# Optimization experiments

Measured on AMD Instinct MI355X. Metric: run time of the kernel, lower is better.

## Reference

```python
import jax, jax.numpy as jnp
import numpy as np

B, S, D, H = 256, 128, 1024, 8
DH = D // H  # per-head dim = input_length / head


def setup_inputs() -> dict:
    key = jax.random.key(0)
    ks = jax.random.split(key, 12)
    code = jax.random.normal(ks[0], (B, S, D), dtype=jnp.float32)
    # 0/1 adjacency (PDG relation mask)
    input_relation = jax.random.bernoulli(ks[1], 0.2, (B, S, S)).astype(jnp.float32)
    w = 0.02
    Wq = jax.random.normal(ks[2], (H, D, DH), dtype=jnp.float32) * w
    bq = jnp.zeros((H, DH), dtype=jnp.float32)
    Wk = jax.random.normal(ks[3], (H, D, DH), dtype=jnp.float32) * w
    bk = jnp.zeros((H, DH), dtype=jnp.float32)
    Wv = jax.random.normal(ks[4], (H, D, DH), dtype=jnp.float32) * w
    bv = jnp.zeros((H, DH), dtype=jnp.float32)
    Wo = jax.random.normal(ks[5], (2 * D, D), dtype=jnp.float32) * w
    bo = jnp.zeros((D,), dtype=jnp.float32)
    return {"code": code, "input_relation": input_relation,
            "Wq": Wq, "bq": bq, "Wk": Wk, "bk": bk,
            "Wv": Wv, "bv": bv, "Wo": Wo, "bo": bo}


def reference(code, input_relation, Wq, bq, Wk, bk, Wv, bv, Wo, bo):
    Hn = Wq.shape[0]
    half = Hn // 2
    Sn = code.shape[1]
    E = jnp.eye(Sn, dtype=code.dtype)
    # Faithful to the TF loop: head i < H/2 sees relation + i*I (the loop
    # reassigns input_relation = this_relation + I each iteration);
    # heads i >= H/2 see the ORIGINAL transposed relation.
    i_idx = jnp.arange(half, dtype=code.dtype)  # [half]
    rel_fwd = input_relation[None] + i_idx[:, None, None, None] * E  # [half,B,S,S]
    rel_t = jnp.swapaxes(input_relation, 1, 2)
    rel_bwd = jnp.broadcast_to(rel_t[None], (Hn - half,) + rel_t.shape)
    rels = jnp.concatenate([rel_fwd, rel_bwd], axis=0)  # [H,B,S,S]

    relu = jax.nn.relu
    Q = relu(jnp.einsum('bsd,hdf->hbsf', code, Wq) + bq[:, None, None, :])
    K = relu(jnp.einsum('bsd,hdf->hbsf', code, Wk) + bk[:, None, None, :])
    V = relu(jnp.einsum('bsd,hdf->hbsf', code, Wv) + bv[:, None, None, :])

    attn = jnp.einsum('hbsf,hbtf->hbst', Q, K)  # [H,B,S,S]
    pdg = rels * attn + 1e-11
    # tf.reduce_sum axis=1 (rows) -> our axis=2; axis=2 (cols) -> our axis=3
    indeg = jnp.sqrt(jnp.sum(pdg, axis=2, keepdims=True))   # [H,B,1,S]
    outdeg = jnp.sqrt(jnp.sum(pdg, axis=3, keepdims=True))  # [H,B,S,1]
    pdg = pdg / indeg / outdeg
    softed = rels * pdg
    res = jnp.einsum('hbst,hbtf->hbsf', softed, V)  # [H,B,S,DH]

    # concat heads along features (head 0 first), then concat original code
    all_ch = jnp.transpose(res, (1, 2, 0, 3)).reshape(code.shape[0], Sn, -1)
    add_ori = jnp.concatenate([all_ch, code], axis=-1)  # [B,S,2D]
    out = relu(add_ori @ Wo + bo)
    return out
```

## Files before the change

kernel.cpp:

```cpp
#include <hip/hip_runtime.h>
#include <cstdint>
#include <cstddef>

#define B_  256
#define S_  128
#define D_  1024
#define H_  8
#define DH_ 128
#define M_  (B_ * S_)

typedef _Float16 half8 __attribute__((ext_vector_type(8)));
typedef float    f32x4 __attribute__((ext_vector_type(4)));

#define GLOAD_LDS16(gp, lp)                                                    \
    __builtin_amdgcn_global_load_lds(                                          \
        (const __attribute__((address_space(1))) void*)(gp),                   \
        (__attribute__((address_space(3))) void*)(lp), 16, 0, 0)

__global__ __launch_bounds__(256)
void cvt_code(const float* __restrict__ src, _Float16* __restrict__ dst, int n8)
{
    int i = blockIdx.x * 256 + threadIdx.x;
    if (i >= n8) return;
    const float4* s = (const float4*)src;
    float4 a = s[2 * i], b = s[2 * i + 1];
    half8 o;
    o[0] = (_Float16)a.x; o[1] = (_Float16)a.y; o[2] = (_Float16)a.z; o[3] = (_Float16)a.w;
    o[4] = (_Float16)b.x; o[5] = (_Float16)b.y; o[6] = (_Float16)b.z; o[7] = (_Float16)b.w;
    *(half8*)(dst + (size_t)i * 8) = o;
}

__global__ __launch_bounds__(256)
void cvt_wqkv(const float* __restrict__ Wq, const float* __restrict__ Wk,
              const float* __restrict__ Wv,
              const float* __restrict__ bq, const float* __restrict__ bk,
              const float* __restrict__ bv,
              _Float16* __restrict__ Wt, float* __restrict__ bias_all)
{
    int idx = blockIdx.x * 256 + threadIdx.x;
    if (idx >= 3072 * 128) return;
    int n = idx >> 7, kc = idx & 127, k = kc * 8;
    int qkv = n >> 10, hf = n & 1023, h = hf >> 7, f = hf & 127;
    const float* W = (qkv == 0 ? Wq : (qkv == 1 ? Wk : Wv))
                     + (size_t)h * D_ * DH_ + (size_t)k * DH_ + f;
    half8 o;
    #pragma unroll
    for (int j = 0; j < 8; ++j) o[j] = (_Float16)W[(size_t)j * DH_];
    *(half8*)(Wt + (size_t)n * 1024 + k) = o;
    if (kc == 0)
        bias_all[n] = (qkv == 0 ? bq : (qkv == 1 ? bk : bv))[h * DH_ + f];
}

__global__ __launch_bounds__(256)
void cvt_wo(const float* __restrict__ Wo, _Float16* __restrict__ Wot)
{
    int idx = blockIdx.x * 256 + threadIdx.x;
    if (idx >= 1024 * 256) return;
    int n = idx >> 8, kc = idx & 255, k = kc * 8;
    const float* W = Wo + (size_t)k * 1024 + n;
    half8 o;
    #pragma unroll
    for (int j = 0; j < 8; ++j) o[j] = (_Float16)W[(size_t)j * 1024];
    *(half8*)(Wot + (size_t)n * 2048 + k) = o;
}

template <bool OUTF32>
__global__ __launch_bounds__(512, 1)
void gemm_f16_8p(const _Float16* __restrict__ A1p, const _Float16* __restrict__ A2p,
                 int K1, const _Float16* __restrict__ Bt,
                 const float* __restrict__ bias, void* __restrict__ outp,
                 int Ntot, int Ktot, int ntn)
{
    __shared__ __align__(16) char lds[131072];

    const int tid = threadIdx.x;
    const int w = tid >> 6, l = tid & 63;
    const int wm = w >> 2, wn = w & 3;
    const int lr = l & 15, lg = l >> 4;

    const int cpx = gridDim.x >> 3;
    const int bid = blockIdx.x;
    const int swz = (bid & 7) * cpx + (bid >> 3);
    const int m0 = (swz / ntn) * 256, n0 = (swz % ntn) * 256;

    const int NT = Ktot >> 6;

    const int srow  = l >> 3;
    const int sgcol = ((l & 7) ^ srow) * 8;

    auto stageHalf = [&](int bufi, int t, int half) {
        const int k0 = t << 6;
        const bool isA = (half == 0) || (half == 3);
        const int hh = (half >= 2) ? 1 : 0;
        char* dst0 = lds + bufi * 65536 + (isA ? 0 : 32768) + hh * 16384;
        if (isA) {
            const _Float16* Asrc; int kc;
            if (k0 < K1) { Asrc = A1p; kc = k0; } else { Asrc = A2p; kc = k0 - K1; }
            #pragma unroll
            for (int i = 0; i < 2; ++i) {
                const int c = i * 8 + w;
                const int row = hh * 128 + c * 8 + srow;
                const _Float16* g = Asrc + (size_t)(m0 + row) * 1024 + kc + sgcol;
                GLOAD_LDS16(g, dst0 + c * 1024);
            }
        } else {
            #pragma unroll
            for (int i = 0; i < 2; ++i) {
                const int c = i * 8 + w;
                const int row = hh * 128 + c * 8 + srow;
                const _Float16* g = Bt + (size_t)(n0 + row) * Ktot + k0 + sgcol;
                GLOAD_LDS16(g, dst0 + c * 1024);
            }
        }
    };

    auto ldA = [&](int bufi, int fi, int ks) -> half8 {
        const int row = fi * 32 + wm * 16 + lr;
        const int pos = (ks * 4 + lg) ^ (row & 7);
        return *(const half8*)(lds + bufi * 65536 + row * 128 + pos * 16);
    };
    auto ldB = [&](int bufi, int fj, int ks) -> half8 {
        const int row = fj * 64 + wn * 16 + lr;
        const int pos = (ks * 4 + lg) ^ (row & 7);
        return *(const half8*)(lds + bufi * 65536 + 32768 + row * 128 + pos * 16);
    };

    f32x4 acc[8][4] = {};
    half8 aq[4][2], b0[2][2], b1[2][2];

    stageHalf(0, 0, 0); stageHalf(0, 0, 1); stageHalf(0, 0, 2); stageHalf(0, 0, 3);

    for (int t = 0; t < NT; ++t) {
        const int buf = t & 1;
        const bool nl = (t + 1 < NT);

        asm volatile("s_waitcnt vmcnt(0)" ::: "memory");
        __builtin_amdgcn_s_barrier();

        if (nl) {
            stageHalf(buf ^ 1, t + 1, 0); stageHalf(buf ^ 1, t + 1, 1);
            stageHalf(buf ^ 1, t + 1, 2); stageHalf(buf ^ 1, t + 1, 3);
        }

        #pragma unroll
        for (int fi = 0; fi < 4; ++fi)
            #pragma unroll
            for (int ks = 0; ks < 2; ++ks)
                aq[fi][ks] = ldA(buf, fi, ks);
        #pragma unroll
        for (int fj = 0; fj < 2; ++fj)
            #pragma unroll
            for (int ks = 0; ks < 2; ++ks)
                b0[fj][ks] = ldB(buf, fj, ks);
        #pragma unroll
        for (int fj = 0; fj < 2; ++fj)
            #pragma unroll
            for (int ks = 0; ks < 2; ++ks)
                b1[fj][ks] = ldB(buf, fj + 2, ks);

        __builtin_amdgcn_s_setprio(1);
        #pragma unroll
        for (int ks = 0; ks < 2; ++ks)
            #pragma unroll
            for (int fi = 0; fi < 4; ++fi)
                #pragma unroll
                for (int fj = 0; fj < 2; ++fj)
                    acc[fi][fj] = __builtin_amdgcn_mfma_f32_16x16x32_f16(
                        aq[fi][ks], b0[fj][ks], acc[fi][fj], 0, 0, 0);
        #pragma unroll
        for (int ks = 0; ks < 2; ++ks)
            #pragma unroll
            for (int fi = 0; fi < 4; ++fi)
                #pragma unroll
                for (int fj = 0; fj < 2; ++fj)
                    acc[fi][fj + 2] = __builtin_amdgcn_mfma_f32_16x16x32_f16(
                        aq[fi][ks], b1[fj][ks], acc[fi][fj + 2], 0, 0, 0);
        __builtin_amdgcn_s_setprio(0);

        __builtin_amdgcn_s_barrier();

        #pragma unroll
        for (int fi = 0; fi < 4; ++fi)
            #pragma unroll
            for (int ks = 0; ks < 2; ++ks)
                aq[fi][ks] = ldA(buf, fi + 4, ks);

        __builtin_amdgcn_s_setprio(1);
        #pragma unroll
        for (int ks = 0; ks < 2; ++ks)
            #pragma unroll
            for (int fi = 0; fi < 4; ++fi)
                #pragma unroll
                for (int fj = 0; fj < 2; ++fj)
                    acc[fi + 4][fj + 2] = __builtin_amdgcn_mfma_f32_16x16x32_f16(
                        aq[fi][ks], b1[fj][ks], acc[fi + 4][fj + 2], 0, 0, 0);
        #pragma unroll
        for (int ks = 0; ks < 2; ++ks)
            #pragma unroll
            for (int fi = 0; fi < 4; ++fi)
                #pragma unroll
                for (int fj = 0; fj < 2; ++fj)
                    acc[fi + 4][fj] = __builtin_amdgcn_mfma_f32_16x16x32_f16(
                        aq[fi][ks], b0[fj][ks], acc[fi + 4][fj], 0, 0, 0);
        __builtin_amdgcn_s_setprio(0);
    }

    #pragma unroll
    for (int fi = 0; fi < 8; ++fi) {
        #pragma unroll
        for (int fj = 0; fj < 4; ++fj) {
            const int n = n0 + fj * 64 + wn * 16 + lr;
            const float bs = bias[n];
            #pragma unroll
            for (int rg = 0; rg < 4; ++rg) {
                const int m = m0 + fi * 32 + wm * 16 + lg * 4 + rg;
                float v = acc[fi][fj][rg] + bs;
                v = v > 0.0f ? v : 0.0f;
                if constexpr (OUTF32)
                    ((float*)outp)[(size_t)m * Ntot + n] = v;
                else
                    ((_Float16*)outp)[(size_t)m * Ntot + n] = (_Float16)v;
            }
        }
    }
}

__global__ __launch_bounds__(256, 2)
void attn_pdg_mfma(const _Float16* __restrict__ QKV, const float* __restrict__ Rel,
                   _Float16* __restrict__ resh)
{
    __shared__ __align__(16) char smem[75776];
    unsigned* rbits = (unsigned*)(smem + 70656);
    float* rowpart  = (float*)(smem + 72704);
    float* colpart  = (float*)(smem + 73728);
    float* inv_in   = (float*)(smem + 74752);
    float* inv_out  = (float*)(smem + 75264);

    const int tid = threadIdx.x;
    const int w = tid >> 6, l = tid & 63;
    const int wr = w >> 1, wc = w & 1;
    const int lr = l & 15, lg = l >> 4;
    const int h = blockIdx.x, b = blockIdx.y;

    for (int s = w; s < S_; s += 4) {
        const float* row = &Rel[((size_t)b * S_ + s) * S_];
        unsigned long long b0m = __ballot(row[l] > 0.5f);
        unsigned long long b1m = __ballot(row[64 + l] > 0.5f);
        if (l == 0) {
            rbits[s * 4 + 0] = (unsigned)b0m; rbits[s * 4 + 1] = (unsigned)(b0m >> 32);
            rbits[s * 4 + 2] = (unsigned)b1m; rbits[s * 4 + 3] = (unsigned)(b1m >> 32);
        }
    }

    const size_t gbase = (size_t)(b * S_) * 3072 + h * DH_;

    const _Float16* Vb = QKV + gbase + 2048;
    const int vrow = tid >> 1, vcol0 = (tid & 1) * 64;
    uint4 vreg[8];
    #pragma unroll
    for (int j = 0; j < 8; ++j)
        vreg[j] = *(const uint4*)&Vb[(size_t)vrow * 3072 + vcol0 + j * 8];

    #pragma unroll
    for (int i = 0; i < 8; ++i) {
        const int row = (w * 8 + i) * 4 + (l >> 4);
        const int gsrc = (l & 15) ^ (row & 7);
        const _Float16* gq = QKV + gbase + (size_t)row * 3072 + gsrc * 8;
        GLOAD_LDS16(gq, smem + (w * 8 + i) * 1024);
        const _Float16* gk = QKV + gbase + 1024 + (size_t)row * 3072 + gsrc * 8;
        GLOAD_LDS16(gk, smem + 32768 + (w * 8 + i) * 1024);
    }
    __syncthreads();

    f32x4 acc[4][4] = {};
    #pragma unroll
    for (int kc = 0; kc < 4; ++kc) {
        half8 af[4], bf[4];
        #pragma unroll
        for (int i = 0; i < 4; ++i) {
            const int row = wr * 64 + i * 16 + lr;
            const int pos = (kc * 4 + lg) ^ (row & 7);
            af[i] = *(const half8*)(smem + row * 256 + pos * 16);
        }
        #pragma unroll
        for (int j = 0; j < 4; ++j) {
            const int row = wc * 64 + j * 16 + lr;
            const int pos = (kc * 4 + lg) ^ (row & 7);
            bf[j] = *(const half8*)(smem + 32768 + row * 256 + pos * 16);
        }
        #pragma unroll
        for (int i = 0; i < 4; ++i)
            #pragma unroll
            for (int j = 0; j < 4; ++j)
                acc[i][j] = __builtin_amdgcn_mfma_f32_16x16x32_f16(af[i], bf[j], acc[i][j], 0, 0, 0);
    }

    auto relf = [&](int s, int t) -> float {
        float r;
        if (h < H_ / 2) {
            r = (float)((rbits[s * 4 + (t >> 5)] >> (t & 31)) & 1u);
            if (s == t) r += (float)h;
        } else {
            r = (float)((rbits[t * 4 + (s >> 5)] >> (s & 31)) & 1u);
        }
        return r;
    };

    f32x4 p[4][4];
    #pragma unroll
    for (int i = 0; i < 4; ++i)
        #pragma unroll
        for (int j = 0; j < 4; ++j)
            #pragma unroll
            for (int rg = 0; rg < 4; ++rg) {
                const int s = wr * 64 + i * 16 + lg * 4 + rg;
                const int t = wc * 64 + j * 16 + lr;
                p[i][j][rg] = relf(s, t) * acc[i][j][rg] + 1e-11f;
            }

    #pragma unroll
    for (int i = 0; i < 4; ++i)
        #pragma unroll
        for (int rg = 0; rg < 4; ++rg) {
            float part = p[i][0][rg] + p[i][1][rg] + p[i][2][rg] + p[i][3][rg];
            part += __shfl_xor(part, 1);
            part += __shfl_xor(part, 2);
            part += __shfl_xor(part, 4);
            part += __shfl_xor(part, 8);
            if (lr == 0) rowpart[wc * 128 + wr * 64 + i * 16 + lg * 4 + rg] = part;
        }
    #pragma unroll
    for (int j = 0; j < 4; ++j) {
        float part = 0.0f;
        #pragma unroll
        for (int i = 0; i < 4; ++i)
            part += p[i][j][0] + p[i][j][1] + p[i][j][2] + p[i][j][3];
        part += __shfl_xor(part, 16);
        part += __shfl_xor(part, 32);
        if (lg == 0) colpart[wr * 128 + wc * 64 + j * 16 + lr] = part;
    }
    __syncthreads();

    if (tid < 128) {
        inv_in[tid] = rsqrtf(colpart[tid] + colpart[128 + tid]);
    } else {
        const int s = tid - 128;
        inv_out[s] = rsqrtf(rowpart[s] + rowpart[128 + s]);
    }
    __syncthreads();

    float itj[4];
    #pragma unroll
    for (int j = 0; j < 4; ++j) itj[j] = inv_in[wc * 64 + j * 16 + lr];
    #pragma unroll
    for (int i = 0; i < 4; ++i)
        #pragma unroll
        for (int rg = 0; rg < 4; ++rg) {
            const int s = wr * 64 + i * 16 + lg * 4 + rg;
            const float os = inv_out[s];
            #pragma unroll
            for (int j = 0; j < 4; ++j) {
                const int t = wc * 64 + j * 16 + lr;
                const float val = relf(s, t) * p[i][j][rg] * itj[j] * os;
                *(_Float16*)(smem + s * 272 + t * 2) = (_Float16)val;
            }
        }

    #pragma unroll
    for (int j = 0; j < 8; ++j) {
        union { uint4 u; _Float16 hh[8]; } uu;
        uu.u = vreg[j];
        #pragma unroll
        for (int e = 0; e < 8; ++e) {
            const int f = vcol0 + j * 8 + e;
            *(_Float16*)(smem + 34816 + f * 280 + vrow * 2) = uu.hh[e];
        }
    }
    __syncthreads();

    f32x4 acc2[4][4] = {};
    #pragma unroll
    for (int kc = 0; kc < 4; ++kc) {
        half8 af[4], bf[4];
        #pragma unroll
        for (int i = 0; i < 4; ++i)
            af[i] = *(const half8*)(smem + (wr * 64 + i * 16 + lr) * 272 + kc * 64 + lg * 16);
        #pragma unroll
        for (int j = 0; j < 4; ++j)
            bf[j] = *(const half8*)(smem + 34816 + (wc * 64 + j * 16 + lr) * 280 + kc * 64 + lg * 16);
        #pragma unroll
        for (int i = 0; i < 4; ++i)
            #pragma unroll
            for (int j = 0; j < 4; ++j)
                acc2[i][j] = __builtin_amdgcn_mfma_f32_16x16x32_f16(af[i], bf[j], acc2[i][j], 0, 0, 0);
    }

    #pragma unroll
    for (int i = 0; i < 4; ++i)
        #pragma unroll
        for (int rg = 0; rg < 4; ++rg) {
            const int s = wr * 64 + i * 16 + lg * 4 + rg;
            #pragma unroll
            for (int j = 0; j < 4; ++j) {
                const int f = wc * 64 + j * 16 + lr;
                resh[((size_t)(b * S_ + s)) * 1024 + h * DH_ + f] = (_Float16)acc2[i][j][rg];
            }
        }
}

extern "C" void kernel_launch(void* const* d_in, const int* in_sizes, int n_in,
                              void* d_out, int out_size, void* d_ws, size_t ws_size,
                              hipStream_t stream)
{
    const float* code = (const float*)d_in[0];
    const float* Rel  = (const float*)d_in[1];
    const float* Wq   = (const float*)d_in[2];
    const float* bq   = (const float*)d_in[3];
    const float* Wk   = (const float*)d_in[4];
    const float* bk   = (const float*)d_in[5];
    const float* Wv   = (const float*)d_in[6];
    const float* bv   = (const float*)d_in[7];
    const float* Wo   = (const float*)d_in[8];
    const float* bo   = (const float*)d_in[9];
    float* out = (float*)d_out;
    (void)in_sizes; (void)n_in; (void)out_size; (void)ws_size;

    char* wsp = (char*)d_ws;
    _Float16* codeh = (_Float16*)wsp;  wsp += (size_t)M_ * 1024 * 2;
    _Float16* QKV   = (_Float16*)wsp;  wsp += (size_t)M_ * 3072 * 2;
    _Float16* resh  = (_Float16*)wsp;  wsp += (size_t)M_ * 1024 * 2;
    _Float16* Wt    = (_Float16*)wsp;  wsp += (size_t)3072 * 1024 * 2;
    _Float16* Wot   = (_Float16*)wsp;  wsp += (size_t)1024 * 2048 * 2;
    float* bias_all = (float*)wsp;     wsp += 3072 * 4;

    cvt_code<<<(M_ * 1024 / 8 + 255) / 256, 256, 0, stream>>>(code, codeh, M_ * 1024 / 8);
    cvt_wqkv<<<(3072 * 128 + 255) / 256, 256, 0, stream>>>(Wq, Wk, Wv, bq, bk, bv, Wt, bias_all);
    cvt_wo<<<(1024 * 256 + 255) / 256, 256, 0, stream>>>(Wo, Wot);

    gemm_f16_8p<false><<<(M_ / 256) * (3072 / 256), 512, 0, stream>>>(
        codeh, codeh, 1024, Wt, bias_all, (void*)QKV, 3072, 1024, 3072 / 256);

    attn_pdg_mfma<<<dim3(H_, B_), 256, 0, stream>>>(QKV, Rel, resh);

    gemm_f16_8p<true><<<(M_ / 256) * (1024 / 256), 512, 0, stream>>>(
        resh, codeh, 1024, Wot, bo, (void*)out, 1024, 2048, 1024 / 256);
}
```

Baseline: 595.0 us.

## Replace 256x256 K64 GEMM with 128x256 K32 tile for higher occupancy

Rewrites both projection GEMMs to use a 128x256 output tile with a K-step of 32, a 48KB LDS double buffer and launch bounds allowing up to 4 blocks per CU. It drops the XOR-swizzled LDS layout and the two-phase MFMA schedule, giving each wave a 4x4 accumulator block. The aim is to raise occupancy and overlap memory with compute across blocks. In exchange it halves per-tile arithmetic intensity, doubles the number of barriers per K, and the unswizzled 64-byte-row LDS reads may cause bank conflicts.

```diff
diff --git a/kernel.cpp b/kernel.cpp
--- a/kernel.cpp
+++ b/kernel.cpp
@@ -65,13 +65,13 @@
 }
 
 template <bool OUTF32>
-__global__ __launch_bounds__(512, 1)
-void gemm_f16_8p(const _Float16* __restrict__ A1p, const _Float16* __restrict__ A2p,
-                 int K1, const _Float16* __restrict__ Bt,
-                 const float* __restrict__ bias, void* __restrict__ outp,
-                 int Ntot, int Ktot, int ntn)
-{
-    __shared__ __align__(16) char lds[131072];
+__global__ __launch_bounds__(512, 4)
+void gemm_f16_b32(const _Float16* __restrict__ A1p, const _Float16* __restrict__ A2p,
+                  int K1, const _Float16* __restrict__ Bt,
+                  const float* __restrict__ bias, void* __restrict__ outp,
+                  int Ntot, int Ktot, int ntn)
+{
+    __shared__ __align__(16) char lds[49152];
 
     const int tid = threadIdx.x;
     const int w = tid >> 6, l = tid & 63;
@@ -81,54 +81,31 @@
     const int cpx = gridDim.x >> 3;
     const int bid = blockIdx.x;
     const int swz = (bid & 7) * cpx + (bid >> 3);
-    const int m0 = (swz / ntn) * 256, n0 = (swz % ntn) * 256;
-
-    const int NT = Ktot >> 6;
-
-    const int srow  = l >> 3;
-    const int sgcol = ((l & 7) ^ srow) * 8;
-
-    auto stageHalf = [&](int bufi, int t, int half) {
-        const int k0 = t << 6;
-        const bool isA = (half == 0) || (half == 3);
-        const int hh = (half >= 2) ? 1 : 0;
-        char* dst0 = lds + bufi * 65536 + (isA ? 0 : 32768) + hh * 16384;
-        if (isA) {
+    const int m0 = (swz / ntn) * 128, n0 = (swz % ntn) * 256;
+
+    const int NT = Ktot >> 5;
+
+    auto stage = [&](int bufi, int t) {
+        const int k0 = t << 5;
+        char* base = lds + bufi * 24576;
+        const int rr = l >> 2, cc = (l & 3) * 8;
+        {
             const _Float16* Asrc; int kc;
             if (k0 < K1) { Asrc = A1p; kc = k0; } else { Asrc = A2p; kc = k0 - K1; }
-            #pragma unroll
-            for (int i = 0; i < 2; ++i) {
-                const int c = i * 8 + w;
-                const int row = hh * 128 + c * 8 + srow;
-                const _Float16* g = Asrc + (size_t)(m0 + row) * 1024 + kc + sgcol;
-                GLOAD_LDS16(g, dst0 + c * 1024);
-            }
-        } else {
-            #pragma unroll
-            for (int i = 0; i < 2; ++i) {
-                const int c = i * 8 + w;
-                const int row = hh * 128 + c * 8 + srow;
-                const _Float16* g = Bt + (size_t)(n0 + row) * Ktot + k0 + sgcol;
-                GLOAD_LDS16(g, dst0 + c * 1024);
-            }
+            const _Float16* g = Asrc + (size_t)(m0 + w * 16 + rr) * 1024 + kc + cc;
+            GLOAD_LDS16(g, base + w * 1024);
+        }
+        #pragma unroll
+        for (int i = 0; i < 2; ++i) {
+            const int row = i * 128 + w * 16 + rr;
+            const _Float16* g = Bt + (size_t)(n0 + row) * Ktot + k0 + cc;
+            GLOAD_LDS16(g, base + 8192 + i * 8192 + w * 1024);
         }
     };
 
-    auto ldA = [&](int bufi, int fi, int ks) -> half8 {
-        const int row = fi * 32 + wm * 16 + lr;
-        const int pos = (ks * 4 + lg) ^ (row & 7);
-        return *(const half8*)(lds + bufi * 65536 + row * 128 + pos * 16);
-    };
-    auto ldB = [&](int bufi, int fj, int ks) -> half8 {
-        const int row = fj * 64 + wn * 16 + lr;
-        const int pos = (ks * 4 + lg) ^ (row & 7);
-        return *(const half8*)(lds + bufi * 65536 + 32768 + row * 128 + pos * 16);
-    };
-
-    f32x4 acc[8][4] = {};
-    half8 aq[4][2], b0[2][2], b1[2][2];
-
-    stageHalf(0, 0, 0); stageHalf(0, 0, 1); stageHalf(0, 0, 2); stageHalf(0, 0, 3);
+    f32x4 acc[4][4] = {};
+
+    stage(0, 0);
 
     for (int t = 0; t < NT; ++t) {
         const int buf = t & 1;
@@ -137,84 +114,36 @@
         asm volatile("s_waitcnt vmcnt(0)" ::: "memory");
         __builtin_amdgcn_s_barrier();
 
-        if (nl) {
-            stageHalf(buf ^ 1, t + 1, 0); stageHalf(buf ^ 1, t + 1, 1);
-            stageHalf(buf ^ 1, t + 1, 2); stageHalf(buf ^ 1, t + 1, 3);
-        }
-
-        #pragma unroll
-        for (int fi = 0; fi < 4; ++fi)
-            #pragma unroll
-            for (int ks = 0; ks < 2; ++ks)
-                aq[fi][ks] = ldA(buf, fi, ks);
-        #pragma unroll
-        for (int fj = 0; fj < 2; ++fj)
-            #pragma unroll
-            for (int ks = 0; ks < 2; ++ks)
-                b0[fj][ks] = ldB(buf, fj, ks);
-        #pragma unroll
-        for (int fj = 0; fj < 2; ++fj)
-            #pragma unroll
-            for (int ks = 0; ks < 2; ++ks)
-                b1[fj][ks] = ldB(buf, fj + 2, ks);
+        if (nl) stage(buf ^ 1, t + 1);
+
+        half8 af[4], bf[4];
+        #pragma unroll
+        for (int i = 0; i < 4; ++i)
+            af[i] = *(const half8*)(lds + buf * 24576 + (wm * 64 + i * 16 + lr) * 64 + lg * 16);
+        #pragma unroll
+        for (int j = 0; j < 4; ++j)
+            bf[j] = *(const half8*)(lds + buf * 24576 + 8192 + (wn * 64 + j * 16 + lr) * 64 + lg * 16);
 
         __builtin_amdgcn_s_setprio(1);
         #pragma unroll
-        for (int ks = 0; ks < 2; ++ks)
-            #pragma unroll
-            for (int fi = 0; fi < 4; ++fi)
-                #pragma unroll
-                for (int fj = 0; fj < 2; ++fj)
-                    acc[fi][fj] = __builtin_amdgcn_mfma_f32_16x16x32_f16(
-                        aq[fi][ks], b0[fj][ks], acc[fi][fj], 0, 0, 0);
-        #pragma unroll
-        for (int ks = 0; ks < 2; ++ks)
-            #pragma unroll
-            for (int fi = 0; fi < 4; ++fi)
-                #pragma unroll
-                for (int fj = 0; fj < 2; ++fj)
-                    acc[fi][fj + 2] = __builtin_amdgcn_mfma_f32_16x16x32_f16(
-                        aq[fi][ks], b1[fj][ks], acc[fi][fj + 2], 0, 0, 0);
+        for (int i = 0; i < 4; ++i)
+            #pragma unroll
+            for (int j = 0; j < 4; ++j)
+                acc[i][j] = __builtin_amdgcn_mfma_f32_16x16x32_f16(
+                    af[i], bf[j], acc[i][j], 0, 0, 0);
         __builtin_amdgcn_s_setprio(0);
-
-        __builtin_amdgcn_s_barrier();
-
-        #pragma unroll
-        for (int fi = 0; fi < 4; ++fi)
-            #pragma unroll
-            for (int ks = 0; ks < 2; ++ks)
-                aq[fi][ks] = ldA(buf, fi + 4, ks);
-
-        __builtin_amdgcn_s_setprio(1);
-        #pragma unroll
-        for (int ks = 0; ks < 2; ++ks)
-            #pragma unroll
-            for (int fi = 0; fi < 4; ++fi)
-                #pragma unroll
-                for (int fj = 0; fj < 2; ++fj)
-                    acc[fi + 4][fj + 2] = __builtin_amdgcn_mfma_f32_16x16x32_f16(
-                        aq[fi][ks], b1[fj][ks], acc[fi + 4][fj + 2], 0, 0, 0);
-        #pragma unroll
-        for (int ks = 0; ks < 2; ++ks)
-            #pragma unroll
-            for (int fi = 0; fi < 4; ++fi)
-                #pragma unroll
-                for (int fj = 0; fj < 2; ++fj)
-                    acc[fi + 4][fj] = __builtin_amdgcn_mfma_f32_16x16x32_f16(
-                        aq[fi][ks], b0[fj][ks], acc[fi + 4][fj], 0, 0, 0);
-        __builtin_amdgcn_s_setprio(0);
-    }
-
-    #pragma unroll
-    for (int fi = 0; fi < 8; ++fi) {
-        #pragma unroll
-        for (int fj = 0; fj < 4; ++fj) {
-            const int n = n0 + fj * 64 + wn * 16 + lr;
+    }
+
+    #pragma unroll
+    for (int i = 0; i < 4; ++i) {
+        #pragma unroll
+        for (int j = 0; j < 4; ++j) {
+            const int n = n0 + wn * 64 + j * 16 + lr;
             const float bs = bias[n];
             #pragma unroll
             for (int rg = 0; rg < 4; ++rg) {
-                const int m = m0 + fi * 32 + wm * 16 + lg * 4 + rg;
-                float v = acc[fi][fj][rg] + bs;
+                const int m = m0 + wm * 64 + i * 16 + lg * 4 + rg;
+                float v = acc[i][j][rg] + bs;
                 v = v > 0.0f ? v : 0.0f;
                 if constexpr (OUTF32)
                     ((float*)outp)[(size_t)m * Ntot + n] = v;
@@ -437,11 +366,11 @@
     cvt_wqkv<<<(3072 * 128 + 255) / 256, 256, 0, stream>>>(Wq, Wk, Wv, bq, bk, bv, Wt, bias_all);
     cvt_wo<<<(1024 * 256 + 255) / 256, 256, 0, stream>>>(Wo, Wot);
 
-    gemm_f16_8p<false><<<(M_ / 256) * (3072 / 256), 512, 0, stream>>>(
+    gemm_f16_b32<false><<<(M_ / 128) * (3072 / 256), 512, 0, stream>>>(
         codeh, codeh, 1024, Wt, bias_all, (void*)QKV, 3072, 1024, 3072 / 256);
 
     attn_pdg_mfma<<<dim3(H_, B_), 256, 0, stream>>>(QKV, Rel, resh);
 
-    gemm_f16_8p<true><<<(M_ / 256) * (1024 / 256), 512, 0, stream>>>(
+    gemm_f16_b32<true><<<(M_ / 128) * (1024 / 256), 512, 0, stream>>>(
         resh, codeh, 1024, Wot, bo, (void*)out, 1024, 2048, 1024 / 256);
 }
```

After: 620.8 us. +4.3%, slower.
